# Performance work log

Hardware: AMD Instinct MI355X
Metric: run time of the kernel (lower is better)

## Reference

```python
import jax, jax.numpy as jnp
import numpy as np

NUM_CAPS = 32
OUT_DIM = 8   # capsule vector length in channel terms; note the view() below mixes spatial dims
H_OUT = 6
W_OUT = 6


def setup_inputs() -> dict:
    key = jax.random.key(0)
    k1, k2, k3 = jax.random.split(key, 3)
    X = jax.random.normal(k1, (512, 256, 20, 20), dtype=jnp.float32)
    # 32 Conv2d(256->8, k=9) stacked capsule-major into one grouped-output conv
    W = jax.random.normal(k2, (256, 256, 9, 9), dtype=jnp.float32) * 0.02
    b = jax.random.normal(k3, (256,), dtype=jnp.float32) * 0.02
    return {"X": X, "W": W, "b": b}


def squash(u):
    # u: [B, 1152, 8]; squash along last dim (matches torch code exactly)
    ns = jnp.sum(u * u, axis=-1, keepdims=True)
    return ns / (1.0 + ns) * (u / (0.001 + jnp.sqrt(ns)))


def reference(X, W, b):
    # One conv replaces the 32 separate Conv2d modules; output channels are
    # ordered [cap0_ch0..cap0_ch7, cap1_ch0..], identical to torch.stack(dim=1)
    # followed by contiguous view.
    y = jax.lax.conv_general_dilated(
        X, W, window_strides=(2, 2), padding='VALID',
        dimension_numbers=('NCHW', 'OIHW', 'NCHW'))  # [B, 256, 6, 6]
    y = y + b[None, :, None, None]
    B = X.shape[0]
    # torch: stack -> [B,32,8,6,6] -> view(B, 32*36, -1) is a raw contiguous
    # reshape; [B,256,6,6] has the same memory layout, so reshape directly.
    u = y.reshape(B, NUM_CAPS * H_OUT * W_OUT, OUT_DIM)  # [B, 1152, 8]
    return squash(u)
```

## Files before the change

### kernel.cpp

```cpp
#include <hip/hip_runtime.h>
#include <hip/hip_bf16.h>
#include <stdint.h>

typedef __attribute__((ext_vector_type(8))) short bf16x8;
typedef __attribute__((ext_vector_type(4))) float f32x4;

__device__ __forceinline__ unsigned short f2bf(float f) {
  union { float f; unsigned int u; } v; v.f = f;
  unsigned int u = v.u;
  u += 0x7fffu + ((u >> 16) & 1u);
  return (unsigned short)(u >> 16);
}

__global__ __launch_bounds__(256) void xform_x(const float* __restrict__ X,
                                               unsigned short* __restrict__ Xt) {
  const int b = blockIdx.x;
  const int t = threadIdx.x;
  const float* src = X + ((size_t)b * 256 + t) * 400;
  unsigned short* dst = Xt + (size_t)b * 400 * 256 + t;
  for (int hw = 0; hw < 400; hw += 4) {
    float4 v = *(const float4*)(src + hw);
    dst[(size_t)(hw + 0) * 256] = f2bf(v.x);
    dst[(size_t)(hw + 1) * 256] = f2bf(v.y);
    dst[(size_t)(hw + 2) * 256] = f2bf(v.z);
    dst[(size_t)(hw + 3) * 256] = f2bf(v.w);
  }
}

__global__ __launch_bounds__(256) void xform_w(const float* __restrict__ W,
                                               unsigned short* __restrict__ Wt) {
  __shared__ unsigned short lds[81 * 128];
  const int co = blockIdx.x;
  const int ct = blockIdx.y;
  const int t = threadIdx.x;
  const float* src = W + ((size_t)co * 256 + (size_t)ct * 128) * 81;
  for (int idx = t; idx < 128 * 81; idx += 256) {
    int ci_l = idx / 81, khw = idx - ci_l * 81;
    lds[khw * 128 + ci_l] = f2bf(src[idx]);
  }
  __syncthreads();
  unsigned short* dst = Wt + (size_t)co * 256 + (size_t)ct * 128;
  for (int idx = t; idx < 81 * 128; idx += 256) {
    int khw = idx >> 7, ci_l = idx & 127;
    dst[(size_t)khw * 65536 + ci_l] = lds[idx];
  }
}

__device__ __forceinline__ void gload16(const unsigned short* g, unsigned short* l) {
  __builtin_amdgcn_global_load_lds(
      (const __attribute__((address_space(1))) unsigned int*)g,
      (__attribute__((address_space(3))) unsigned int*)l, 16, 0, 0);
}

__global__ __launch_bounds__(256, 2) void conv_gemm(
    const unsigned short* __restrict__ Xt,
    const unsigned short* __restrict__ Wt,
    const float* __restrict__ bias,
    float* __restrict__ Y) {
  __shared__ unsigned short sA[128 * 64];
  __shared__ unsigned short sB[64 * 64];
  const int mt = blockIdx.x;
  const int nt = blockIdx.y;
  const int t = threadIdx.x;
  const int c8 = t & 7, rq = t >> 3;
  const int swz = (c8 ^ (rq & 7)) * 8;

  int xb[4];
  #pragma unroll
  for (int r = 0; r < 4; ++r) {
    int m = mt * 128 + r * 32 + rq;
    int b = m / 36, s = m - b * 36;
    int oh = s / 6, ow = s - oh * 6;
    xb[r] = ((b * 20 + 2 * oh) * 20 + 2 * ow) * 256;
  }
  int wb[2];
  #pragma unroll
  for (int r = 0; r < 2; ++r) wb[r] = (nt * 64 + r * 32 + rq) * 256;

  unsigned short* ldsA = sA + t * 8;
  unsigned short* ldsB = sB + t * 8;

  const int lane = t & 63, wv = t >> 6;
  const int wm = (wv >> 1) * 64, wn = (wv & 1) * 32;
  const int l15 = lane & 15, l4 = lane >> 4, l7 = lane & 7;

  const unsigned short* pA[4][2];
  const unsigned short* pB[2][2];
  #pragma unroll
  for (int i = 0; i < 4; ++i)
    #pragma unroll
    for (int kk = 0; kk < 2; ++kk)
      pA[i][kk] = sA + ((wm + i * 16 + l15) * 128 +
                        ((kk * 64 + l4 * 16) ^ (l7 << 4))) / 2;
  #pragma unroll
  for (int j = 0; j < 2; ++j)
    #pragma unroll
    for (int kk = 0; kk < 2; ++kk)
      pB[j][kk] = sB + ((wn + j * 16 + l15) * 128 +
                        ((kk * 64 + l4 * 16) ^ (l7 << 4))) / 2;

  f32x4 acc[4][2];
  #pragma unroll
  for (int i = 0; i < 4; ++i)
    #pragma unroll
    for (int j = 0; j < 2; ++j) acc[i][j] = (f32x4){0.f, 0.f, 0.f, 0.f};

  #pragma unroll 1
  for (int kh = 0; kh < 9; ++kh) {
    #pragma unroll 1
    for (int kw = 0; kw < 9; ++kw) {
      const unsigned short* xsrc = Xt + (kh * 20 + kw) * 256 + swz;
      const unsigned short* wsrc = Wt + (kh * 9 + kw) * 65536 + swz;
      for (int ci0 = 0; ci0 < 256; ci0 += 64) {
        gload16(xsrc + xb[0] + ci0, ldsA + 0 * 2048);
        gload16(xsrc + xb[1] + ci0, ldsA + 1 * 2048);
        gload16(xsrc + xb[2] + ci0, ldsA + 2 * 2048);
        gload16(xsrc + xb[3] + ci0, ldsA + 3 * 2048);
        gload16(wsrc + wb[0] + ci0, ldsB + 0 * 2048);
        gload16(wsrc + wb[1] + ci0, ldsB + 1 * 2048);
        __syncthreads();
        bf16x8 af[4][2], bfr[2][2];
        #pragma unroll
        for (int i = 0; i < 4; ++i)
          #pragma unroll
          for (int kk = 0; kk < 2; ++kk) af[i][kk] = *(const bf16x8*)pA[i][kk];
        #pragma unroll
        for (int j = 0; j < 2; ++j)
          #pragma unroll
          for (int kk = 0; kk < 2; ++kk) bfr[j][kk] = *(const bf16x8*)pB[j][kk];
        #pragma unroll
        for (int i = 0; i < 4; ++i)
          #pragma unroll
          for (int j = 0; j < 2; ++j) {
            acc[i][j] = __builtin_amdgcn_mfma_f32_16x16x32_bf16(
                af[i][0], bfr[j][0], acc[i][j], 0, 0, 0);
            acc[i][j] = __builtin_amdgcn_mfma_f32_16x16x32_bf16(
                af[i][1], bfr[j][1], acc[i][j], 0, 0, 0);
          }
        __syncthreads();
      }
    }
  }

  #pragma unroll
  for (int j = 0; j < 2; ++j) {
    int co = nt * 64 + wn + j * 16 + l15;
    float bb = bias[co];
    #pragma unroll
    for (int i = 0; i < 4; ++i) {
      int m0 = mt * 128 + wm + i * 16 + l4 * 4;
      #pragma unroll
      for (int q = 0; q < 4; ++q) {
        int m = m0 + q;
        int b = m / 36, s = m - b * 36;
        Y[((size_t)b * 256 + co) * 36 + s] = acc[i][j][q] + bb;
      }
    }
  }
}

__global__ __launch_bounds__(256) void squash_k(float* __restrict__ Y) {
  const int g = blockIdx.x * 256 + threadIdx.x;
  float4* p = (float4*)(Y + (size_t)g * 8);
  float4 a = p[0], b = p[1];
  float ns = a.x * a.x + a.y * a.y + a.z * a.z + a.w * a.w +
             b.x * b.x + b.y * b.y + b.z * b.z + b.w * b.w;
  float sc = ns / ((1.0f + ns) * (0.001f + sqrtf(ns)));
  a.x *= sc; a.y *= sc; a.z *= sc; a.w *= sc;
  b.x *= sc; b.y *= sc; b.z *= sc; b.w *= sc;
  p[0] = a; p[1] = b;
}

extern "C" void kernel_launch(void* const* d_in, const int* in_sizes, int n_in,
                              void* d_out, int out_size, void* d_ws, size_t ws_size,
                              hipStream_t stream) {
  const float* X = (const float*)d_in[0];
  const float* W = (const float*)d_in[1];
  const float* bias = (const float*)d_in[2];
  float* Y = (float*)d_out;

  unsigned short* Xt = (unsigned short*)d_ws;
  unsigned short* Wt = Xt + (size_t)512 * 400 * 256;

  xform_x<<<512, 256, 0, stream>>>(X, Xt);
  xform_w<<<dim3(256, 2), 256, 0, stream>>>(W, Wt);
  conv_gemm<<<dim3(144, 4), 256, 0, stream>>>(Xt, Wt, bias, Y);
  squash_k<<<2304, 256, 0, stream>>>(Y);
}
```

Measured before the change: 385.0 us.

## Restructure conv GEMM: 2 waves, 32x32 MFMA, B from registers, flattened K loop

The conv GEMM drops to 128 threads (2 waves), each wave covering 64 rows by all 64 output channels with 32x32x16 bf16 MFMAs. Weight fragments are now loaded straight from global memory into registers and double-buffered, so only the input tile goes through LDS. The kh/kw/ci loops are flattened into one 324-step loop with incremental offsets. The aim is fewer LDS round trips and larger MFMA tiles, at the cost of more registers, fewer waves per block, and extra barriers per step.

```diff
diff --git a/kernel.cpp b/kernel.cpp
--- a/kernel.cpp
+++ b/kernel.cpp
@@ -3,7 +3,7 @@
 #include <stdint.h>
 
 typedef __attribute__((ext_vector_type(8))) short bf16x8;
-typedef __attribute__((ext_vector_type(4))) float f32x4;
+typedef __attribute__((ext_vector_type(16))) float f32x16;
 
 __device__ __forceinline__ unsigned short f2bf(float f) {
   union { float f; unsigned int u; } v; v.f = f;
@@ -52,108 +52,119 @@
       (__attribute__((address_space(3))) unsigned int*)l, 16, 0, 0);
 }
 
-__global__ __launch_bounds__(256, 2) void conv_gemm(
+__global__ __launch_bounds__(128, 2) void conv_gemm(
     const unsigned short* __restrict__ Xt,
     const unsigned short* __restrict__ Wt,
     const float* __restrict__ bias,
     float* __restrict__ Y) {
-  __shared__ unsigned short sA[128 * 64];
-  __shared__ unsigned short sB[64 * 64];
+  __shared__ __align__(16) unsigned short sA[128 * 64];
   const int mt = blockIdx.x;
   const int nt = blockIdx.y;
   const int t = threadIdx.x;
   const int c8 = t & 7, rq = t >> 3;
   const int swz = (c8 ^ (rq & 7)) * 8;
 
-  int xb[4];
-  #pragma unroll
-  for (int r = 0; r < 4; ++r) {
-    int m = mt * 128 + r * 32 + rq;
+  int xb[8];
+  #pragma unroll
+  for (int r = 0; r < 8; ++r) {
+    int m = mt * 128 + r * 16 + rq;
     int b = m / 36, s = m - b * 36;
     int oh = s / 6, ow = s - oh * 6;
-    xb[r] = ((b * 20 + 2 * oh) * 20 + 2 * ow) * 256;
-  }
-  int wb[2];
-  #pragma unroll
-  for (int r = 0; r < 2; ++r) wb[r] = (nt * 64 + r * 32 + rq) * 256;
-
-  unsigned short* ldsA = sA + t * 8;
-  unsigned short* ldsB = sB + t * 8;
-
-  const int lane = t & 63, wv = t >> 6;
-  const int wm = (wv >> 1) * 64, wn = (wv & 1) * 32;
-  const int l15 = lane & 15, l4 = lane >> 4, l7 = lane & 7;
-
-  const unsigned short* pA[4][2];
-  const unsigned short* pB[2][2];
-  #pragma unroll
-  for (int i = 0; i < 4; ++i)
-    #pragma unroll
-    for (int kk = 0; kk < 2; ++kk)
-      pA[i][kk] = sA + ((wm + i * 16 + l15) * 128 +
-                        ((kk * 64 + l4 * 16) ^ (l7 << 4))) / 2;
-  #pragma unroll
-  for (int j = 0; j < 2; ++j)
-    #pragma unroll
-    for (int kk = 0; kk < 2; ++kk)
-      pB[j][kk] = sB + ((wn + j * 16 + l15) * 128 +
-                        ((kk * 64 + l4 * 16) ^ (l7 << 4))) / 2;
-
-  f32x4 acc[4][2];
-  #pragma unroll
-  for (int i = 0; i < 4; ++i)
-    #pragma unroll
-    for (int j = 0; j < 2; ++j) acc[i][j] = (f32x4){0.f, 0.f, 0.f, 0.f};
-
-  #pragma unroll 1
-  for (int kh = 0; kh < 9; ++kh) {
-    #pragma unroll 1
-    for (int kw = 0; kw < 9; ++kw) {
-      const unsigned short* xsrc = Xt + (kh * 20 + kw) * 256 + swz;
-      const unsigned short* wsrc = Wt + (kh * 9 + kw) * 65536 + swz;
-      for (int ci0 = 0; ci0 < 256; ci0 += 64) {
-        gload16(xsrc + xb[0] + ci0, ldsA + 0 * 2048);
-        gload16(xsrc + xb[1] + ci0, ldsA + 1 * 2048);
-        gload16(xsrc + xb[2] + ci0, ldsA + 2 * 2048);
-        gload16(xsrc + xb[3] + ci0, ldsA + 3 * 2048);
-        gload16(wsrc + wb[0] + ci0, ldsB + 0 * 2048);
-        gload16(wsrc + wb[1] + ci0, ldsB + 1 * 2048);
-        __syncthreads();
-        bf16x8 af[4][2], bfr[2][2];
-        #pragma unroll
-        for (int i = 0; i < 4; ++i)
-          #pragma unroll
-          for (int kk = 0; kk < 2; ++kk) af[i][kk] = *(const bf16x8*)pA[i][kk];
+    xb[r] = ((b * 20 + 2 * oh) * 20 + 2 * ow) * 256 + swz;
+  }
+  const int dA = t * 8;
+
+  const int l = t & 63, w = t >> 6;
+  const int r31 = l & 31, ch = l >> 5;
+
+  int aOff[2][4];
+  #pragma unroll
+  for (int i = 0; i < 2; ++i)
+    #pragma unroll
+    for (int kk = 0; kk < 4; ++kk)
+      aOff[i][kk] = (w * 64 + i * 32 + r31) * 64 + (((kk * 2 + ch) ^ (r31 & 7)) * 8);
+
+  int vB[2];
+  #pragma unroll
+  for (int j = 0; j < 2; ++j) vB[j] = (nt * 64 + j * 32 + r31) * 256 + ch * 8;
+
+  f32x16 acc[2][2];
+  #pragma unroll
+  for (int i = 0; i < 2; ++i)
+    #pragma unroll
+    for (int j = 0; j < 2; ++j) acc[i][j] = (f32x16)(0.f);
+
+  int ciX = 0, kwX = 0, xo = 0;
+  int ciW = 0, wo = 0;
+  auto advX = [&]() {
+    if (ciX < 3) { ++ciX; xo += 64; }
+    else { ciX = 0;
+           if (kwX < 8) { ++kwX; xo += 64; }
+           else         { kwX = 0; xo += 2880; } }
+  };
+  auto advW = [&]() {
+    if (ciW < 3) { ++ciW; wo += 64; }
+    else { ciW = 0; wo += 65536 - 192; }
+  };
+  auto stage = [&]() {
+    #pragma unroll
+    for (int r = 0; r < 8; ++r) gload16(Xt + xb[r] + xo, sA + dA + r * 1024);
+    advX();
+  };
+  auto loadB = [&](bf16x8 (&bf)[2][4]) {
+    const unsigned short* base = Wt + wo;
+    #pragma unroll
+    for (int j = 0; j < 2; ++j)
+      #pragma unroll
+      for (int kk = 0; kk < 4; ++kk)
+        bf[j][kk] = *(const bf16x8*)(base + vB[j] + kk * 16);
+    advW();
+  };
+  auto compute = [&](bf16x8 (&bf)[2][4]) {
+    bf16x8 fa[2][4];
+    #pragma unroll
+    for (int i = 0; i < 2; ++i)
+      #pragma unroll
+      for (int kk = 0; kk < 4; ++kk) fa[i][kk] = *(const bf16x8*)(sA + aOff[i][kk]);
+    #pragma unroll
+    for (int kk = 0; kk < 4; ++kk)
+      #pragma unroll
+      for (int i = 0; i < 2; ++i)
         #pragma unroll
         for (int j = 0; j < 2; ++j)
-          #pragma unroll
-          for (int kk = 0; kk < 2; ++kk) bfr[j][kk] = *(const bf16x8*)pB[j][kk];
-        #pragma unroll
-        for (int i = 0; i < 4; ++i)
-          #pragma unroll
-          for (int j = 0; j < 2; ++j) {
-            acc[i][j] = __builtin_amdgcn_mfma_f32_16x16x32_bf16(
-                af[i][0], bfr[j][0], acc[i][j], 0, 0, 0);
-            acc[i][j] = __builtin_amdgcn_mfma_f32_16x16x32_bf16(
-                af[i][1], bfr[j][1], acc[i][j], 0, 0, 0);
-          }
-        __syncthreads();
-      }
-    }
+          acc[i][j] = __builtin_amdgcn_mfma_f32_32x32x16_bf16(
+              fa[i][kk], bf[j][kk], acc[i][j], 0, 0, 0);
+  };
+
+  bf16x8 b0[2][4], b1[2][4];
+  loadB(b0);
+  stage();
+  #pragma unroll 1
+  for (int s = 0; s < 324; s += 2) {
+    __syncthreads();
+    loadB(b1);
+    compute(b0);
+    __syncthreads();
+    stage();
+    __syncthreads();
+    if (s + 2 < 324) loadB(b0);
+    compute(b1);
+    __syncthreads();
+    if (s + 2 < 324) stage();
   }
 
   #pragma unroll
   for (int j = 0; j < 2; ++j) {
-    int co = nt * 64 + wn + j * 16 + l15;
+    int co = nt * 64 + j * 32 + r31;
     float bb = bias[co];
     #pragma unroll
-    for (int i = 0; i < 4; ++i) {
-      int m0 = mt * 128 + wm + i * 16 + l4 * 4;
-      #pragma unroll
-      for (int q = 0; q < 4; ++q) {
-        int m = m0 + q;
+    for (int i = 0; i < 2; ++i) {
+      #pragma unroll
+      for (int e = 0; e < 16; ++e) {
+        int row = (e & 3) + 8 * (e >> 2) + 4 * ch;
+        int m = mt * 128 + w * 64 + i * 32 + row;
         int b = m / 36, s = m - b * 36;
-        Y[((size_t)b * 256 + co) * 36 + s] = acc[i][j][q] + bb;
+        Y[((size_t)b * 256 + co) * 36 + s] = acc[i][j][e] + bb;
       }
     }
   }
@@ -184,6 +195,6 @@
 
   xform_x<<<512, 256, 0, stream>>>(X, Xt);
   xform_w<<<dim3(256, 2), 256, 0, stream>>>(W, Wt);
-  conv_gemm<<<dim3(144, 4), 256, 0, stream>>>(Xt, Wt, bias, Y);
+  conv_gemm<<<dim3(144, 4), 128, 0, stream>>>(Xt, Wt, bias, Y);
   squash_k<<<2304, 256, 0, stream>>>(Y);
 }
```

Result: slower. 699.7 us (+81.8%).
